# Performance work log

Measured on AMD Instinct MI355X. Metric: run time of the kernel, lower is better.

## Reference

```python
import jax, jax.numpy as jnp
import numpy as np

T, B, D, H = 32, 128, 256, 768
MAX_PONDER = 8
EPS = 0.01


def setup_inputs() -> dict:
    key = jax.random.key(0)
    ks = jax.random.split(key, 6)
    s = 1.0 / np.sqrt(H)
    return {
        "input_": jax.random.normal(ks[0], (T, B, D), jnp.float32),
        "W_ih": jax.random.uniform(ks[1], (H, D + 1), jnp.float32, -s, s),
        "W_hh": jax.random.uniform(ks[2], (H, H), jnp.float32, -s, s),
        "b_ih": jax.random.uniform(ks[3], (H,), jnp.float32, -s, s),
        "b_hh": jax.random.uniform(ks[4], (H,), jnp.float32, -s, s),
        "w_p": jax.random.uniform(ks[5], (H,), jnp.float32, -s, s),
        "b_p": jnp.ones((1,), jnp.float32),  # torch reset_parameters fills ponder bias with 1
    }


def reference(input_, W_ih, W_hh, b_ih, b_hh, w_p, b_p):
    T_, B_, D_ = input_.shape
    H_ = W_hh.shape[0]
    dt = input_.dtype
    hx0 = jnp.zeros((B_, H_), dt)

    def time_step(carry, x_t):
        hx, pcost = carry

        def ponder(c, _):
            hx_i, ah, ahx, sc, spc, mask, flag = c
            # input row with ponder flag (0 on first act step, 1 afterwards)
            x_in = jnp.concatenate([x_t, jnp.full((B_, 1), flag, dt)], axis=1)
            # ponder cost assigned for active rows before update
            spc = jnp.where(mask, -ah, spc)
            hx_new = jnp.tanh(x_in @ W_ih.T + b_ih + hx_i @ W_hh.T + b_hh)
            hx_i = jnp.where(mask[:, None], hx_new, hx_i)
            mf = mask.astype(dt)
            ahx = ahx + mf[:, None] * hx_new  # accum_hx += hx (as in source)
            h = jax.nn.sigmoid(hx_new @ w_p + b_p[0])
            ah2 = ah + mf * h
            p = h - jnp.maximum(ah2 - 1.0, 0.0)
            ahx = ahx + (mf * p)[:, None] * hx_new  # accum_hx += p*hx
            sc = sc + mf
            mask2 = ah2 < (1.0 - EPS)
            return (hx_i, ah2, ahx, sc, spc, mask2, jnp.ones((), dt)), None

        init = (hx,
                jnp.zeros((B_,), dt),           # accum_h
                jnp.zeros((B_, H_), dt),        # accum_hx
                jnp.zeros((B_,), dt),           # step_count
                jnp.zeros((B_,), dt),           # step_ponder_cost
                jnp.ones((B_,), bool),          # selector
                jnp.zeros((), dt))              # flag
        (hx_i, ah, ahx, sc, spc, mask, flag), _ = jax.lax.scan(
            ponder, init, None, length=MAX_PONDER)
        hx_out = ahx / sc[:, None]
        return (hx_out, pcost + spc), (hx_out, sc)

    (hx_last, pcost), (all_hx, steps) = jax.lax.scan(
        time_step, (hx0, jnp.zeros((B_,), dt)), input_)
    # all_hx: [T,B,H], hx: [1,B,H], ponder_cost: [B], ponder_times: [T,B]
    return all_hx, hx_last[None], pcost, steps
```

## Files before the change

kernel.cpp:

```cpp
#include <hip/hip_runtime.h>
#include <math.h>

#define TT 32
#define BB 128
#define DD 256
#define HH 768
#define MAXP 8

#define RG   8
#define RPG  16
#define CB   12
#define CS   64
#define NTH  256
#define NCH  24

#define OFF_LAST  ((size_t)TT * BB * HH)
#define OFF_PCOST (OFF_LAST + (size_t)BB * HH)
#define OFF_STEPS (OFF_PCOST + BB)

#define ASCOPE __HIP_MEMORY_SCOPE_AGENT

typedef __attribute__((ext_vector_type(8))) short s16x8;
typedef __attribute__((ext_vector_type(4))) float f32x4;
typedef unsigned long long ull;

static __device__ __forceinline__ unsigned short f2bf(float f) {
    unsigned u = __float_as_uint(f);
    u = (u + 0x7fffu + ((u >> 16) & 1u)) >> 16;
    return (unsigned short)u;
}
static __device__ __forceinline__ float bf2f(unsigned short h) {
    return __uint_as_float(((unsigned)h) << 16);
}
static __device__ __forceinline__ float fast_tanh(float v) {
    return 1.f - 2.f / (__expf(2.f * v) + 1.f);
}

union AU { float4 f; s16x8 s; unsigned short e[8]; };

__launch_bounds__(NTH, 1)
__global__ void act_kernel(const float* __restrict__ x,
                           const float* __restrict__ Wih,
                           const float* __restrict__ Whh,
                           const float* __restrict__ bih,
                           const float* __restrict__ bhh,
                           const float* __restrict__ wpv,
                           const float* __restrict__ bp,
                           float* __restrict__ out,
                           unsigned* __restrict__ flags,
                           s16x8* __restrict__ hxe,
                           float* __restrict__ zpt)
{
    const int tid  = threadIdx.x;
    const int rg   = blockIdx.x & 7;
    const int cbk  = blockIdx.x >> 3;
    const int r0   = rg * RPG;
    const int c0   = cbk * CS;
    const int CT   = tid >> 6;
    const int lane = tid & 63;
    const int am   = lane & 15;
    const int aq   = lane >> 4;

    __shared__ s16x8 A_s[NCH * 64];
    __shared__ s16x8 WB_s[4 * 8 * 64];
    __shared__ s16x8 xA_s[8 * 64];
    __shared__ unsigned short hxn_s[RPG][72];
    __shared__ float wp_s[CS];

    s16x8 Breg[NCH];
    {
        const float* wr = Whh + (size_t)(c0 + CT*16 + am) * HH + aq*8;
        for (int ch = 0; ch < NCH; ++ch) {
            float4 a0 = *(const float4*)(wr + ch*32);
            float4 a1 = *(const float4*)(wr + ch*32 + 4);
            union { s16x8 v; unsigned short e[8]; } u;
            u.e[0]=f2bf(a0.x); u.e[1]=f2bf(a0.y); u.e[2]=f2bf(a0.z); u.e[3]=f2bf(a0.w);
            u.e[4]=f2bf(a1.x); u.e[5]=f2bf(a1.y); u.e[6]=f2bf(a1.z); u.e[7]=f2bf(a1.w);
            Breg[ch] = u.v;
        }
    }
    for (int ch = 0; ch < 8; ++ch) {
        const float* wr = Wih + (size_t)(c0 + CT*16 + am) * (DD+1) + ch*32 + aq*8;
        union { s16x8 v; unsigned short e[8]; } u;
        #pragma unroll
        for (int j = 0; j < 8; ++j) u.e[j] = f2bf(wr[j]);
        WB_s[(CT*8 + ch)*64 + lane] = u.v;
    }
    if (tid < CS) wp_s[tid] = wpv[c0 + tid];
    const int myc = c0 + CT*16 + am;
    const float bs_lane = bih[myc] + bhh[myc];
    const float wfl     = Wih[(size_t)myc*(DD+1) + DD];
    const float bp0     = bp[0];
    {
        s16x8 z8 = {0,0,0,0,0,0,0,0};
        #pragma unroll
        for (int j = 0; j < 6; ++j) A_s[j*NTH + tid] = z8;
    }

    float pc = 0.f;
    unsigned it = 0;

    for (int t = 0; t < TT; ++t) {
        #pragma unroll
        for (int j = 0; j < 2; ++j) {
            const int s = j*NTH + tid;
            const int ch = s >> 6;
            const float* xb = x + ((size_t)t*BB + r0 + am)*DD + ch*32 + aq*8;
            float4 a0 = *(const float4*)xb;
            float4 a1 = *(const float4*)(xb + 4);
            union { s16x8 v; unsigned short e[8]; } u;
            u.e[0]=f2bf(a0.x); u.e[1]=f2bf(a0.y); u.e[2]=f2bf(a0.z); u.e[3]=f2bf(a0.w);
            u.e[4]=f2bf(a1.x); u.e[5]=f2bf(a1.y); u.e[6]=f2bf(a1.z); u.e[7]=f2bf(a1.w);
            xA_s[s] = u.v;
        }
        __syncthreads();

        f32x4 xi;
        {
            f32x4 a = {0.f,0.f,0.f,0.f};
            #pragma unroll
            for (int ch = 0; ch < 8; ++ch)
                a = __builtin_amdgcn_mfma_f32_16x16x32_bf16(
                        xA_s[ch*64 + lane], WB_s[(CT*8 + ch)*64 + lane], a, 0, 0, 0);
            xi[0]=a[0]+bs_lane; xi[1]=a[1]+bs_lane; xi[2]=a[2]+bs_lane; xi[3]=a[3]+bs_lane;
        }

        float ahx[48];
        #pragma unroll
        for (int q = 0; q < 48; ++q) ahx[q] = 0.f;
        float ah = 0.f, sc = 0.f, spc = 0.f;
        int act = 1;

        {
            f32x4 acc = xi;
            #pragma unroll
            for (int ch = 0; ch < NCH; ++ch)
                acc = __builtin_amdgcn_mfma_f32_16x16x32_bf16(
                        A_s[ch*64 + lane], Breg[ch], acc, 0, 0, 0);
            #pragma unroll
            for (int r = 0; r < 4; ++r)
                hxn_s[aq*4 + r][CT*16 + am] = f2bf(fast_tanh(acc[r]));
        }
        __syncthreads();

        for (int pk = 1; ; ++pk) {
            const unsigned par = it & 1u;

            if (CT == 0) {
                ull*   exw = (ull*)(hxe + (size_t)(rg*2 + par) * (NCH*64));
                float* zpw = zpt + (size_t)(rg*2 + par) * (RPG*CB);
                const ull* s0 = (const ull*)&hxn_s[am][aq*8];
                const ull* s1 = (const ull*)&hxn_s[am][32 + aq*8];
                ull* d0 = exw + ((size_t)(2*cbk)*64   + lane)*2;
                ull* d1 = exw + ((size_t)(2*cbk+1)*64 + lane)*2;
                __hip_atomic_store(d0,   s0[0], __ATOMIC_RELAXED, ASCOPE);
                __hip_atomic_store(d0+1, s0[1], __ATOMIC_RELAXED, ASCOPE);
                __hip_atomic_store(d1,   s1[0], __ATOMIC_RELAXED, ASCOPE);
                __hip_atomic_store(d1+1, s1[1], __ATOMIC_RELAXED, ASCOPE);
                const int zr = lane >> 2, zc = lane & 3;
                float sz = 0.f;
                #pragma unroll
                for (int i = 0; i < 16; ++i)
                    sz += bf2f(hxn_s[zr][zc*16 + i]) * wp_s[zc*16 + i];
                sz += __shfl_xor(sz, 1);
                sz += __shfl_xor(sz, 2);
                if (zc == 0)
                    __hip_atomic_store(&zpw[zr*CB + cbk], sz, __ATOMIC_RELAXED, ASCOPE);
                __builtin_amdgcn_fence(__ATOMIC_RELEASE, "agent");
                if (lane == 0)
                    __hip_atomic_store(&flags[rg*16 + cbk], it + 1u, __ATOMIC_RELAXED, ASCOPE);
                const int pi = lane % 12;
                unsigned v;
                do { v = __hip_atomic_load(&flags[rg*16 + pi], __ATOMIC_RELAXED, ASCOPE); }
                while (!__all((int)(v >= it + 1u)));
                __builtin_amdgcn_fence(__ATOMIC_ACQUIRE, "agent");
            }
            ++it;
            __syncthreads();

            const s16x8* exr = hxe + (size_t)(rg*2 + par) * (NCH*64);
            const float* zpr = zpt + (size_t)(rg*2 + par) * (RPG*CB);

            const float4* zb4 = (const float4*)(zpr + am*CB);
            const float4 z0 = zb4[0], z1 = zb4[1], z2 = zb4[2];
            AU aload[NCH];
            #pragma unroll
            for (int ch = 0; ch < NCH; ++ch)
                aload[ch].f = *(const float4*)&exr[ch*64 + lane];

            const float z = ((z0.x+z0.y)+(z0.z+z0.w))
                          + ((z1.x+z1.y)+(z1.z+z1.w))
                          + ((z2.x+z2.y)+(z2.z+z2.w));
            const float h = 1.f / (1.f + __expf(-(z + bp0)));
            float w1 = 0.f;
            if (act) {
                spc = -ah;
                ah += h;
                w1 = 1.f + (h - fmaxf(ah - 1.f, 0.f));
                sc += 1.f;
                act = (ah < 0.99f) ? 1 : 0;
            }
            const bool done = __all(act == 0) || (pk == MAXP);

            if (done) {
                #pragma unroll
                for (int ch = 0; ch < NCH; ++ch)
                    if ((ch & 3) == CT) {
                        const int j = ch >> 2;
                        #pragma unroll
                        for (int i = 0; i < 8; ++i)
                            ahx[j*8 + i] += w1 * bf2f(aload[ch].e[i]);
                    }
                break;
            }

            f32x4 acc = xi;
            #pragma unroll
            for (int ch = 0; ch < NCH; ++ch)
                acc = __builtin_amdgcn_mfma_f32_16x16x32_bf16(
                        aload[ch].s, Breg[ch], acc, 0, 0, 0);
            #pragma unroll
            for (int ch = 0; ch < NCH; ++ch)
                if ((ch & 3) == CT) {
                    const int j = ch >> 2;
                    #pragma unroll
                    for (int i = 0; i < 8; ++i)
                        ahx[j*8 + i] += w1 * bf2f(aload[ch].e[i]);
                }
            #pragma unroll
            for (int r = 0; r < 4; ++r)
                hxn_s[aq*4 + r][CT*16 + am] = f2bf(fast_tanh(acc[r] + wfl));
            __syncthreads();
        }

        const float inv = 1.f / sc;
        pc += spc;
        if (cbk == 0 && tid < RPG) out[OFF_STEPS + (size_t)t*BB + r0 + tid] = sc;
        #pragma unroll
        for (int j = 0; j < 6; ++j) {
            const int ch = j*4 + CT;
            float o[8];
            #pragma unroll
            for (int i = 0; i < 8; ++i) o[i] = ahx[j*8 + i] * inv;
            union { s16x8 v; unsigned short e[8]; } u;
            #pragma unroll
            for (int i = 0; i < 8; ++i) u.e[i] = f2bf(o[i]);
            A_s[ch*64 + lane] = u.v;
            if (cbk == 0) {
                float* op = out + ((size_t)t*BB + r0 + am)*HH + ch*32 + aq*8;
                *(float4*)op       = make_float4(o[0], o[1], o[2], o[3]);
                *(float4*)(op + 4) = make_float4(o[4], o[5], o[6], o[7]);
                if (t == TT-1) {
                    float* lp = out + OFF_LAST + (size_t)(r0 + am)*HH + ch*32 + aq*8;
                    *(float4*)lp       = make_float4(o[0], o[1], o[2], o[3]);
                    *(float4*)(lp + 4) = make_float4(o[4], o[5], o[6], o[7]);
                }
            }
        }
    }
    if (cbk == 0 && tid < RPG) out[OFF_PCOST + r0 + tid] = pc;
}

extern "C" void kernel_launch(void* const* d_in, const int* in_sizes, int n_in,
                              void* d_out, int out_size, void* d_ws, size_t ws_size,
                              hipStream_t stream) {
    const float* x   = (const float*)d_in[0];
    const float* Wih = (const float*)d_in[1];
    const float* Whh = (const float*)d_in[2];
    const float* bih = (const float*)d_in[3];
    const float* bhh = (const float*)d_in[4];
    const float* wpv = (const float*)d_in[5];
    const float* bp  = (const float*)d_in[6];
    float* out = (float*)d_out;

    unsigned* flags = (unsigned*)d_ws;
    s16x8*    hxe   = (s16x8*)((char*)d_ws + 4096);
    float*    zpt   = (float*)((char*)d_ws + 4096 + (size_t)RG*2*NCH*64*16);

    hipMemsetAsync(d_ws, 0, 4096, stream);
    act_kernel<<<dim3(RG*CB), dim3(NTH), 0, stream>>>(
        x, Wih, Whh, bih, bhh, wpv, bp, out, flags, hxe, zpt);
}
```

Measured before the change: 431.0 us.

## Split publish from wait, share exchanged hidden state across waves via LDS

The exchange publish (global stores of the new hidden tile and partial ponder dot) moves into a lambda called right after each hidden update, so the flag-wait loop is separated from the publish. Instead of every wave loading all 24 chunks from global memory, each wave now loads only its 6 chunks with atomic loads and writes them into shared memory, and the MFMA reads operands from LDS after an extra barrier. The release/acquire fences are replaced with an explicit s_waitcnt vmcnt(0) before the flag store and no acquire fence after the wait. This cuts redundant global traffic per ponder step, but adds a block barrier and relies on relaxed loads plus waitcnt for cross-block ordering, which may be weaker than the previous fences.

After: 352.4 us. 18.2% less time.

```diff
diff --git a/kernel.cpp b/kernel.cpp
--- a/kernel.cpp
+++ b/kernel.cpp
@@ -35,8 +35,6 @@
 static __device__ __forceinline__ float fast_tanh(float v) {
     return 1.f - 2.f / (__expf(2.f * v) + 1.f);
 }
-
-union AU { float4 f; s16x8 s; unsigned short e[8]; };
 
 __launch_bounds__(NTH, 1)
 __global__ void act_kernel(const float* __restrict__ x,
@@ -100,6 +98,35 @@
     float pc = 0.f;
     unsigned it = 0;
 
+    auto publish = [&]() {
+        const unsigned par = it & 1u;
+        if (CT == 0) {
+            ull*   exw = (ull*)(hxe + (size_t)(rg*2 + par) * (NCH*64));
+            float* zpw = zpt + (size_t)(rg*2 + par) * (RPG*CB);
+            const ull* s0 = (const ull*)&hxn_s[am][aq*8];
+            const ull* s1 = (const ull*)&hxn_s[am][32 + aq*8];
+            ull* d0 = exw + ((size_t)(2*cbk)*64   + lane)*2;
+            ull* d1 = exw + ((size_t)(2*cbk+1)*64 + lane)*2;
+            __hip_atomic_store(d0,   s0[0], __ATOMIC_RELAXED, ASCOPE);
+            __hip_atomic_store(d0+1, s0[1], __ATOMIC_RELAXED, ASCOPE);
+            __hip_atomic_store(d1,   s1[0], __ATOMIC_RELAXED, ASCOPE);
+            __hip_atomic_store(d1+1, s1[1], __ATOMIC_RELAXED, ASCOPE);
+            const int zr = lane >> 2, zc = lane & 3;
+            float sz = 0.f;
+            #pragma unroll
+            for (int i = 0; i < 16; ++i)
+                sz += bf2f(hxn_s[zr][zc*16 + i]) * wp_s[zc*16 + i];
+            sz += __shfl_xor(sz, 1);
+            sz += __shfl_xor(sz, 2);
+            if (zc == 0)
+                __hip_atomic_store(&zpw[zr*CB + cbk], sz, __ATOMIC_RELAXED, ASCOPE);
+            asm volatile("s_waitcnt vmcnt(0)" ::: "memory");
+            if (lane == 0)
+                __hip_atomic_store(&flags[rg*16 + cbk], it + 1u, __ATOMIC_RELAXED, ASCOPE);
+        }
+        ++it;
+    };
+
     for (int t = 0; t < TT; ++t) {
         #pragma unroll
         for (int j = 0; j < 2; ++j) {
@@ -142,56 +169,53 @@
                 hxn_s[aq*4 + r][CT*16 + am] = f2bf(fast_tanh(acc[r]));
         }
         __syncthreads();
+        publish();
 
         for (int pk = 1; ; ++pk) {
-            const unsigned par = it & 1u;
-
             if (CT == 0) {
-                ull*   exw = (ull*)(hxe + (size_t)(rg*2 + par) * (NCH*64));
-                float* zpw = zpt + (size_t)(rg*2 + par) * (RPG*CB);
-                const ull* s0 = (const ull*)&hxn_s[am][aq*8];
-                const ull* s1 = (const ull*)&hxn_s[am][32 + aq*8];
-                ull* d0 = exw + ((size_t)(2*cbk)*64   + lane)*2;
-                ull* d1 = exw + ((size_t)(2*cbk+1)*64 + lane)*2;
-                __hip_atomic_store(d0,   s0[0], __ATOMIC_RELAXED, ASCOPE);
-                __hip_atomic_store(d0+1, s0[1], __ATOMIC_RELAXED, ASCOPE);
-                __hip_atomic_store(d1,   s1[0], __ATOMIC_RELAXED, ASCOPE);
-                __hip_atomic_store(d1+1, s1[1], __ATOMIC_RELAXED, ASCOPE);
-                const int zr = lane >> 2, zc = lane & 3;
-                float sz = 0.f;
-                #pragma unroll
-                for (int i = 0; i < 16; ++i)
-                    sz += bf2f(hxn_s[zr][zc*16 + i]) * wp_s[zc*16 + i];
-                sz += __shfl_xor(sz, 1);
-                sz += __shfl_xor(sz, 2);
-                if (zc == 0)
-                    __hip_atomic_store(&zpw[zr*CB + cbk], sz, __ATOMIC_RELAXED, ASCOPE);
-                __builtin_amdgcn_fence(__ATOMIC_RELEASE, "agent");
-                if (lane == 0)
-                    __hip_atomic_store(&flags[rg*16 + cbk], it + 1u, __ATOMIC_RELAXED, ASCOPE);
                 const int pi = lane % 12;
                 unsigned v;
                 do { v = __hip_atomic_load(&flags[rg*16 + pi], __ATOMIC_RELAXED, ASCOPE); }
-                while (!__all((int)(v >= it + 1u)));
-                __builtin_amdgcn_fence(__ATOMIC_ACQUIRE, "agent");
-            }
-            ++it;
+                while (!__all((int)(v >= it)));
+            }
             __syncthreads();
 
-            const s16x8* exr = hxe + (size_t)(rg*2 + par) * (NCH*64);
-            const float* zpr = zpt + (size_t)(rg*2 + par) * (RPG*CB);
-
-            const float4* zb4 = (const float4*)(zpr + am*CB);
-            const float4 z0 = zb4[0], z1 = zb4[1], z2 = zb4[2];
-            AU aload[NCH];
-            #pragma unroll
-            for (int ch = 0; ch < NCH; ++ch)
-                aload[ch].f = *(const float4*)&exr[ch*64 + lane];
-
-            const float z = ((z0.x+z0.y)+(z0.z+z0.w))
-                          + ((z1.x+z1.y)+(z1.z+z1.w))
-                          + ((z2.x+z2.y)+(z2.z+z2.w));
-            const float h = 1.f / (1.f + __expf(-(z + bp0)));
+            const unsigned parR = (it - 1u) & 1u;
+            const ull*   exr = (const ull*)(hxe + (size_t)(rg*2 + parR) * (NCH*64));
+            const float* zpr = zpt + (size_t)(rg*2 + parR) * (RPG*CB);
+
+            ull clo[6], chi[6];
+            #pragma unroll
+            for (int j = 0; j < 6; ++j) {
+                const ull* src = exr + ((size_t)((j*4 + CT)*64 + lane))*2;
+                clo[j] = __hip_atomic_load(src,     __ATOMIC_RELAXED, ASCOPE);
+                chi[j] = __hip_atomic_load(src + 1, __ATOMIC_RELAXED, ASCOPE);
+            }
+            ull zu[6];
+            {
+                const ull* zb = (const ull*)(zpr + am*CB);
+                #pragma unroll
+                for (int j = 0; j < 6; ++j)
+                    zu[j] = __hip_atomic_load(zb + j, __ATOMIC_RELAXED, ASCOPE);
+            }
+            #pragma unroll
+            for (int j = 0; j < 6; ++j) {
+                union { ull u[2]; s16x8 v; } cv;
+                cv.u[0] = clo[j]; cv.u[1] = chi[j];
+                A_s[(j*4 + CT)*64 + lane] = cv.v;
+            }
+
+            float zf[12];
+            #pragma unroll
+            for (int j = 0; j < 6; ++j) {
+                zf[2*j]   = __uint_as_float((unsigned)(zu[j] & 0xffffffffu));
+                zf[2*j+1] = __uint_as_float((unsigned)(zu[j] >> 32));
+            }
+            const float zA = (zf[0]+zf[1]) + (zf[2]+zf[3]);
+            const float zB = (zf[4]+zf[5]) + (zf[6]+zf[7]);
+            const float zC = (zf[8]+zf[9]) + (zf[10]+zf[11]);
+            const float z  = (zA + zB) + zC;
+            const float h  = 1.f / (1.f + __expf(-(z + bp0)));
             float w1 = 0.f;
             if (act) {
                 spc = -ah;
@@ -204,33 +228,35 @@
 
             if (done) {
                 #pragma unroll
-                for (int ch = 0; ch < NCH; ++ch)
-                    if ((ch & 3) == CT) {
-                        const int j = ch >> 2;
-                        #pragma unroll
-                        for (int i = 0; i < 8; ++i)
-                            ahx[j*8 + i] += w1 * bf2f(aload[ch].e[i]);
+                for (int j = 0; j < 6; ++j) {
+                    #pragma unroll
+                    for (int i = 0; i < 4; ++i) {
+                        ahx[j*8 + i]     += w1 * bf2f((unsigned short)(clo[j] >> (16*i)));
+                        ahx[j*8 + 4 + i] += w1 * bf2f((unsigned short)(chi[j] >> (16*i)));
                     }
+                }
                 break;
             }
+            __syncthreads();
 
             f32x4 acc = xi;
             #pragma unroll
             for (int ch = 0; ch < NCH; ++ch)
                 acc = __builtin_amdgcn_mfma_f32_16x16x32_bf16(
-                        aload[ch].s, Breg[ch], acc, 0, 0, 0);
-            #pragma unroll
-            for (int ch = 0; ch < NCH; ++ch)
-                if ((ch & 3) == CT) {
-                    const int j = ch >> 2;
-                    #pragma unroll
-                    for (int i = 0; i < 8; ++i)
-                        ahx[j*8 + i] += w1 * bf2f(aload[ch].e[i]);
+                        A_s[ch*64 + lane], Breg[ch], acc, 0, 0, 0);
+            #pragma unroll
+            for (int j = 0; j < 6; ++j) {
+                #pragma unroll
+                for (int i = 0; i < 4; ++i) {
+                    ahx[j*8 + i]     += w1 * bf2f((unsigned short)(clo[j] >> (16*i)));
+                    ahx[j*8 + 4 + i] += w1 * bf2f((unsigned short)(chi[j] >> (16*i)));
                 }
+            }
             #pragma unroll
             for (int r = 0; r < 4; ++r)
                 hxn_s[aq*4 + r][CT*16 + am] = f2bf(fast_tanh(acc[r] + wfl));
             __syncthreads();
+            publish();
         }
 
         const float inv = 1.f / sc;
```
